# Kernel tuning notes

Hardware: AMD Instinct MI355X
Metric: run time of the kernel (lower is better)

Reference implementation:

```python
import jax, jax.numpy as jnp
import numpy as np

N = 50000
E = 1600000
IN_DIM = 128
OUT_DIM = 128
HEADS = 4
C = OUT_DIM // HEADS  # per-head channels = 32
EDGE_DIM = 16
NEG_SLOPE = 0.2
LN_EPS = 1e-5


def setup_inputs() -> dict:
    key = jax.random.key(0)
    ks = jax.random.split(key, 12)
    s = 1.0 / np.sqrt(IN_DIM)
    return {
        "x": jax.random.normal(ks[0], (N, IN_DIM), dtype=jnp.float32),
        "edge_index": jax.random.randint(ks[1], (2, E), 0, N, dtype=jnp.int64),
        "edge_attr": jax.random.normal(ks[2], (E, EDGE_DIM), dtype=jnp.float32),
        # GATv2Conv params
        "W_l": jax.random.normal(ks[3], (IN_DIM, HEADS * C), dtype=jnp.float32) * s,
        "b_l": jnp.zeros((HEADS * C,), dtype=jnp.float32),
        "W_r": jax.random.normal(ks[4], (IN_DIM, HEADS * C), dtype=jnp.float32) * s,
        "b_r": jnp.zeros((HEADS * C,), dtype=jnp.float32),
        "W_e": jax.random.normal(ks[5], (EDGE_DIM, HEADS * C), dtype=jnp.float32) * (1.0 / np.sqrt(EDGE_DIM)),
        "att": jax.random.normal(ks[6], (HEADS, C), dtype=jnp.float32) * (1.0 / np.sqrt(C)),
        "conv_bias": jnp.zeros((HEADS * C,), dtype=jnp.float32),
        # LayerNorm params
        "gamma": jnp.ones((OUT_DIM,), dtype=jnp.float32),
        "beta": jnp.zeros((OUT_DIM,), dtype=jnp.float32),
    }


def _gat_layer(x, edge_index, edge_attr, W_l, b_l, W_r, b_r, W_e, att, conv_bias, gamma, beta):
    src, dst = edge_index[0], edge_index[1]
    # linear projections -> [N, H, C] / [E, H, C]
    x_l = (x @ W_l + b_l).reshape(N, HEADS, C)  # source-side
    x_r = (x @ W_r + b_r).reshape(N, HEADS, C)  # target-side
    e_f = (edge_attr @ W_e).reshape(E, HEADS, C)
    # GATv2 attention logits per edge/head
    z = x_l[src] + x_r[dst] + e_f                      # [E, H, C]
    z = jnp.where(z >= 0, z, NEG_SLOPE * z)            # LeakyReLU(0.2)
    logits = jnp.einsum('ehc,hc->eh', z, att)          # [E, H]
    # segment softmax over incoming edges of each target node
    m = jax.ops.segment_max(logits, dst, num_segments=N)          # [N, H]
    m = jnp.where(jnp.isfinite(m), m, 0.0)
    ex = jnp.exp(logits - m[dst])                                  # [E, H]
    denom = jax.ops.segment_sum(ex, dst, num_segments=N)          # [N, H]
    alpha = ex / (denom[dst] + 1e-16)                              # [E, H]
    # weighted message aggregation (dropout on alpha skipped: eval mode)
    msg = x_l[src] * alpha[:, :, None]                             # [E, H, C]
    out = jax.ops.segment_sum(msg, dst, num_segments=N)           # [N, H, C]
    out = out.reshape(N, HEADS * C) + conv_bias                    # concat heads
    # LayerNorm -> ReLU -> (dropout: identity) -> residual (Identity since in==out)
    mu = jnp.mean(out, axis=-1, keepdims=True)
    var = jnp.mean(jnp.square(out - mu), axis=-1, keepdims=True)
    out = (out - mu) * jax.lax.rsqrt(var + LN_EPS) * gamma + beta
    out = jax.nn.relu(out)
    return out + x


def reference(x, edge_index, edge_attr, W_l, b_l, W_r, b_r, W_e, att, conv_bias, gamma, beta):
    return _gat_layer(x, edge_index, edge_attr, W_l, b_l, W_r, b_r, W_e, att, conv_bias, gamma, beta)
```

## Files before the change

kernel.cpp:

```cpp
#include <hip/hip_runtime.h>
#include <hip/hip_bf16.h>

#define NPB 32
#define PAD 64
#define OVF_CAP 4096

typedef float f32x2 __attribute__((ext_vector_type(2)));

__device__ __forceinline__ float b2f(__hip_bfloat16 v) { return __bfloat162float(v); }
__device__ __forceinline__ float ldf(const void* p, long i, int f32) {
    return f32 ? ((const float*)p)[i] : b2f(((const __hip_bfloat16*)p)[i]);
}
__device__ __forceinline__ float bflo(unsigned u) { union { unsigned i; float f; } v; v.i = u << 16; return v.f; }
__device__ __forceinline__ float bfhi(unsigned u) { union { unsigned i; float f; } v; v.i = u & 0xffff0000u; return v.f; }
__device__ __forceinline__ float2 ldf2(const void* p, long i2, int f32) {
    if (f32) return ((const float2*)p)[i2];
    unsigned u = ((const unsigned*)p)[i2];
    return make_float2(bflo(u), bfhi(u));
}
__device__ __forceinline__ int ldi(const int* p, long i, int i32) {
    return i32 ? p[i] : p[2 * i];
}
__device__ __forceinline__ int rfl(int v) { return __builtin_amdgcn_readfirstlane(v); }

template <int CTRL>
__device__ __forceinline__ float dpp_add(float v) {
    int s = __builtin_amdgcn_update_dpp(0, __float_as_int(v), CTRL, 0xF, 0xF, true);
    return v + __int_as_float(s);
}

__global__ void zero_i(int* __restrict__ a, long n, int* __restrict__ dt)
{
    long i = (long)blockIdx.x * 256 + threadIdx.x;
    long stride = (long)gridDim.x * 256;
    for (; i < n; i += stride) a[i] = 0;
    if (blockIdx.x == 0 && threadIdx.x == 0 && dt) { dt[0] = 0; dt[1] = 0; }
}

__global__ void fail_stamp(float* __restrict__ out, float code)
{
    if (threadIdx.x == 0 && blockIdx.x == 0) out[0] = code;
}

__global__ void detect_kernel(const void* __restrict__ x, const int* __restrict__ ei,
                              int* __restrict__ dt, int E_)
{
    int t = threadIdx.x;
    const unsigned short* xb = (const unsigned short*)x;
    int f32 = 0;
    for (int i = t; i < 4096; i += 256) {
        int ex = (xb[i] >> 7) & 0xFF;
        if (ex > 140) f32 = 1;
    }
    if (f32) atomicOr(&dt[0], 1);
    int nz = 0;
    for (int i = t; i < 2048; i += 256) nz |= ei[2 * i + 1];
    if (nz) atomicOr(&dt[1], 1);
}

__global__ __launch_bounds__(128) void gemm_xlr(
    const void* __restrict__ x,
    const void* __restrict__ Wl, const void* __restrict__ bl,
    const void* __restrict__ Wr, const void* __restrict__ br,
    const int* __restrict__ dt,
    __hip_bfloat16* __restrict__ xl, __hip_bfloat16* __restrict__ xr, int n)
{
    __shared__ float xs[NPB][128];
    int f32 = dt[0];
    int t = threadIdx.x;
    int n0 = blockIdx.x * NPB;
    for (int j = 0; j < NPB; ++j) {
        int node = n0 + j;
        xs[j][t] = (node < n) ? ldf(x, (long)node * 128 + t, f32) : 0.f;
    }
    __syncthreads();
    f32x2 acc[NPB];
#pragma unroll
    for (int j = 0; j < NPB; ++j) acc[j] = (f32x2){0.f, 0.f};
    for (int k = 0; k < 128; ++k) {
        f32x2 wlr = { ldf(Wl, k * 128 + t, f32), ldf(Wr, k * 128 + t, f32) };
#pragma unroll
        for (int j = 0; j < NPB; ++j) {
            f32x2 xv = { xs[j][k], xs[j][k] };
            acc[j] = __builtin_elementwise_fma(xv, wlr, acc[j]);
        }
    }
    float blv = ldf(bl, t, f32);
    float brv = ldf(br, t, f32);
    for (int j = 0; j < NPB; ++j) {
        int node = n0 + j;
        if (node < n) {
            xl[(long)node * 128 + t] = __float2bfloat16(acc[j].x + blv);
            xr[(long)node * 128 + t] = __float2bfloat16(acc[j].y + brv);
        }
    }
}

__global__ __launch_bounds__(256) void scatter_pad(
    const int* __restrict__ ei, const int* __restrict__ dt,
    int* __restrict__ cnt, int* __restrict__ ovfcnt,
    int2* __restrict__ se_pad, int4* __restrict__ ovf, int E_, int N_)
{
    long e = (long)blockIdx.x * 256 + threadIdx.x;
    if (e >= E_) return;
    int i32 = dt[1];
    int s = ldi(ei, e, i32);
    int d = ldi(ei, E_ + e, i32);
    if ((unsigned)s < (unsigned)N_ && (unsigned)d < (unsigned)N_) {
        int k = atomicAdd(&cnt[d], 1);
        if (k < PAD) se_pad[(long)d * PAD + k] = make_int2(s, (int)e);
        else {
            int o = atomicAdd(ovfcnt, 1);
            if (o < OVF_CAP) ovf[o] = make_int4(d, s, (int)e, 0);
        }
    }
}

#define EDGE_PRE(UC)  f32x2 z = { bflo(UC) + w0, bfhi(UC) + w1 };
#define EFMA(val, idx) z = __builtin_elementwise_fma((f32x2){(val), (val)}, W[idx], z);
#define EDGE_POST(UC) \
    z = __builtin_elementwise_max(z, z * 0.2f);                    \
    float vv = fmaf(z.y, attv.y, z.x * attv.x);                                        \
    vv = dpp_add<0xB1>(vv);  vv = dpp_add<0x4E>(vv);                                   \
    vv = dpp_add<0x124>(vv); vv = dpp_add<0x128>(vv);            \
    float exv = __expf(vv);                                                            \
    acc = __builtin_elementwise_fma((f32x2){exv, exv},                                 \
                                    (f32x2){bflo(UC), bfhi(UC)}, acc);                 \
    den += exv;
#define EDGE16(E0, E1, UC) { EDGE_PRE(UC)                                              \
    EFMA(bflo(E0.x), 0)  EFMA(bfhi(E0.x), 1)  EFMA(bflo(E0.y), 2)  EFMA(bfhi(E0.y), 3) \
    EFMA(bflo(E0.z), 4)  EFMA(bfhi(E0.z), 5)  EFMA(bflo(E0.w), 6)  EFMA(bfhi(E0.w), 7) \
    EFMA(bflo(E1.x), 8)  EFMA(bfhi(E1.x), 9)  EFMA(bflo(E1.y), 10) EFMA(bfhi(E1.y), 11)\
    EFMA(bflo(E1.z), 12) EFMA(bfhi(E1.z), 13) EFMA(bflo(E1.w), 14) EFMA(bfhi(E1.w), 15)\
    EDGE_POST(UC) }
#define EDGE32(F0, F1, F2, F3, UC) { EDGE_PRE(UC)                                      \
    EFMA(F0.x, 0)  EFMA(F0.y, 1)  EFMA(F0.z, 2)  EFMA(F0.w, 3)                          \
    EFMA(F1.x, 4)  EFMA(F1.y, 5)  EFMA(F1.z, 6)  EFMA(F1.w, 7)                          \
    EFMA(F2.x, 8)  EFMA(F2.y, 9)  EFMA(F2.z, 10) EFMA(F2.w, 11)                         \
    EFMA(F3.x, 12) EFMA(F3.y, 13) EFMA(F3.z, 14) EFMA(F3.w, 15)                         \
    EDGE_POST(UC) }

template <int F32>
__device__ __forceinline__ void node_run(
    const int* __restrict__ cnt, const int2* __restrict__ se_pad,
    const int4* __restrict__ ovf, const int* __restrict__ ovfcnt,
    const void* __restrict__ ea, const void* __restrict__ We, const void* __restrict__ att,
    const unsigned* __restrict__ xlu, const unsigned* __restrict__ xru,
    const void* __restrict__ cb, const void* __restrict__ gamma,
    const void* __restrict__ beta, const void* __restrict__ x,
    float* __restrict__ out, int N_)
{
    int w = threadIdx.x >> 6, j = threadIdx.x & 63;
    int n = blockIdx.x * 4 + w;
    if (n >= N_) return;

    f32x2 W[16];
#pragma unroll
    for (int k = 0; k < 16; ++k) {
        float2 v = ldf2(We, (long)k * 64 + j, F32);
        W[k] = (f32x2){v.x, v.y};
    }
    float2 attv = ldf2(att, j, F32);
    float2 cbv  = ldf2(cb, j, F32);
    float2 gv   = ldf2(gamma, j, F32);
    float2 bv   = ldf2(beta, j, F32);

    int deg = cnt[n];
    int m = deg < PAD ? deg : PAD;
    long base = (long)n * PAD;
    unsigned urow = xru[(long)n * 64 + j];
    float w0 = bflo(urow), w1 = bfhi(urow);
    f32x2 acc = {0.f, 0.f};
    float den = 0.f;

    if (m > 0) {
        if (F32) {
            int2 se0 = se_pad[base];
            int sA = rfl(se0.x), eA = rfl(se0.y);
            unsigned uA = xlu[((long)sA << 6) + j];
            const float4* qa = (const float4*)ea + (long)eA * 4;
            float4 f0 = qa[0], f1 = qa[1], f2 = qa[2], f3 = qa[3];
            int2 seB = se_pad[base + (m > 1 ? 1 : 0)];
            for (int k = 0; k < m; ++k) {
                int2 seC = se_pad[base + (k + 2 < m ? k + 2 : m - 1)];
                int sB = rfl(seB.x), eB = rfl(seB.y);
                unsigned uB = xlu[((long)sB << 6) + j];
                const float4* qb = (const float4*)ea + (long)eB * 4;
                float4 g0 = qb[0], g1 = qb[1], g2 = qb[2], g3 = qb[3];
                EDGE32(f0, f1, f2, f3, uA)
                seB = seC; uA = uB; f0 = g0; f1 = g1; f2 = g2; f3 = g3;
            }
        } else {
            int2 se0 = se_pad[base];
            int sA = rfl(se0.x), eA = rfl(se0.y);
            unsigned uA = xlu[((long)sA << 6) + j];
            const uint4* qa = (const uint4*)ea + (long)eA * 2;
            uint4 a0 = qa[0], a1 = qa[1];
            int2 seB = se_pad[base + (m > 1 ? 1 : 0)];
            for (int k = 0; k < m; ++k) {
                int2 seC = se_pad[base + (k + 2 < m ? k + 2 : m - 1)];
                int sB = rfl(seB.x), eB = rfl(seB.y);
                unsigned uB = xlu[((long)sB << 6) + j];
                const uint4* qb = (const uint4*)ea + (long)eB * 2;
                uint4 b0 = qb[0], b1 = qb[1];
                EDGE16(a0, a1, uA)
                seB = seC; uA = uB; a0 = b0; a1 = b1;
            }
        }
    }
    if (deg > PAD) {
        int oc = *ovfcnt; if (oc > OVF_CAP) oc = OVF_CAP;
        for (int o = 0; o < oc; ++o) {
            int4 v4 = ovf[o];
            if (rfl(v4.x) != n) continue;
            int sO = rfl(v4.y); long eO = rfl(v4.z);
            unsigned uO = xlu[((long)sO << 6) + j];
            if (F32) {
                const float4* qr = (const float4*)ea + eO * 4;
                float4 f0 = qr[0], f1 = qr[1], f2 = qr[2], f3 = qr[3];
                EDGE32(f0, f1, f2, f3, uO)
            } else {
                const uint4* qr = (const uint4*)ea + eO * 2;
                uint4 a0 = qr[0], a1 = qr[1];
                EDGE16(a0, a1, uO)
            }
        }
    }

    float rden = 1.f / (den + 1e-16f);
    float o0 = acc.x * rden + cbv.x;
    float o1 = acc.y * rden + cbv.y;

    float s = o0 + o1;
#pragma unroll
    for (int o = 1; o < 64; o <<= 1) s += __shfl_xor(s, o, 64);
    float mu = s * (1.f / 128.f);
    float d0 = o0 - mu, d1 = o1 - mu;
    float vs = d0 * d0 + d1 * d1;
#pragma unroll
    for (int o = 1; o < 64; o <<= 1) vs += __shfl_xor(vs, o, 64);
    float rs = rsqrtf(vs * (1.f / 128.f) + 1e-5f);
    float2 xv = ldf2(x, (long)n * 64 + j, F32);
    float y0 = fmaxf(d0 * rs * gv.x + bv.x, 0.f) + xv.x;
    float y1 = fmaxf(d1 * rs * gv.y + bv.y, 0.f) + xv.y;
    *(float2*)(out + (long)n * 128 + 2 * j) = make_float2(y0, y1);
}

__global__ __launch_bounds__(256, 4) void node_fused(
    const int* __restrict__ cnt, const int2* __restrict__ se_pad,
    const int4* __restrict__ ovf, const int* __restrict__ ovfcnt,
    const void* __restrict__ ea, const void* __restrict__ We, const void* __restrict__ att,
    const __hip_bfloat16* __restrict__ xl, const __hip_bfloat16* __restrict__ xr,
    const void* __restrict__ cb, const void* __restrict__ gamma,
    const void* __restrict__ beta, const void* __restrict__ x,
    const int* __restrict__ dt, float* __restrict__ out, int N_)
{
    const unsigned* xlu = (const unsigned*)xl;
    const unsigned* xru = (const unsigned*)xr;
    if (dt[0])
        node_run<1>(cnt, se_pad, ovf, ovfcnt, ea, We, att, xlu, xru,
                    cb, gamma, beta, x, out, N_);
    else
        node_run<0>(cnt, se_pad, ovf, ovfcnt, ea, We, att, xlu, xru,
                    cb, gamma, beta, x, out, N_);
}

extern "C" void kernel_launch(void* const* d_in, const int* in_sizes, int n_in,
                              void* d_out, int out_size, void* d_ws, size_t ws_size,
                              hipStream_t stream) {
    const void* x     = d_in[0];
    const int*  ei    = (const int*)d_in[1];
    const void* ea    = d_in[2];
    const void* Wl    = d_in[3];
    const void* bl    = d_in[4];
    const void* Wr    = d_in[5];
    const void* br    = d_in[6];
    const void* We    = d_in[7];
    const void* att   = d_in[8];
    const void* cb    = d_in[9];
    const void* gamma = d_in[10];
    const void* beta  = d_in[11];
    float* out = (float*)d_out;

    const int N_ = in_sizes[0] / 128;
    const int E_ = in_sizes[2] / 16;

    size_t need = 0;
    auto sz = [&](size_t b) { size_t r = need; need += (b + 255) & ~(size_t)255; return r; };
    size_t o_xl   = sz((size_t)N_ * 128 * 2);
    size_t o_xr   = sz((size_t)N_ * 128 * 2);
    size_t o_cnt  = sz((size_t)(N_ + 8) * 4);
    size_t o_dt   = sz(256);
    size_t o_se   = sz((size_t)N_ * PAD * 8);
    size_t o_ovf  = sz((size_t)OVF_CAP * 16);

    if (need > ws_size) {
        fail_stamp<<<1, 64, 0, stream>>>(out, 16384.f);
        return;
    }
    char* p = (char*)d_ws;
    __hip_bfloat16* xl   = (__hip_bfloat16*)(p + o_xl);
    __hip_bfloat16* xr   = (__hip_bfloat16*)(p + o_xr);
    int*   cnt           = (int*)(p + o_cnt);
    int*   ovfcnt        = cnt + N_;
    int*   dt            = (int*)(p + o_dt);
    int2*  se_pad        = (int2*)(p + o_se);
    int4*  ovf           = (int4*)(p + o_ovf);

    zero_i<<<256, 256, 0, stream>>>(cnt, N_ + 8, dt);
    detect_kernel<<<1, 256, 0, stream>>>(x, ei, dt, E_);
    gemm_xlr<<<(N_ + NPB - 1) / NPB, 128, 0, stream>>>(x, Wl, bl, Wr, br, dt, xl, xr, N_);
    scatter_pad<<<(E_ + 255) / 256, 256, 0, stream>>>(ei, dt, cnt, ovfcnt,
                                                      se_pad, ovf, E_, N_);
    node_fused<<<(N_ + 3) / 4, 256, 0, stream>>>(cnt, se_pad, ovf, ovfcnt, ea, We, att,
                                                 xl, xr, cb, gamma, beta, x, dt, out, N_);
}
```

Baseline: 620.8 us.

## Merge GEMM and edge scatter into one launch, deepen edge prefetch

Merges the x@W_l/W_r projection and the edge scatter into a single prep kernel, with separate blocks doing each task so they run concurrently. The GEMM now reads x straight from global memory instead of staging it in shared memory, and each thread computes one output column for 16 nodes. The scatter batches four edges per thread so their atomics are in flight together. The node loop prefetches edge data two edges ahead, and an asm constraint keeps W in registers, at the cost of higher register pressure.

```diff
diff --git a/kernel.cpp b/kernel.cpp
--- a/kernel.cpp
+++ b/kernel.cpp
@@ -1,7 +1,7 @@
 #include <hip/hip_runtime.h>
 #include <hip/hip_bf16.h>
 
-#define NPB 32
+#define GJB 16
 #define PAD 64
 #define OVF_CAP 4096
 
@@ -58,61 +58,90 @@
     if (nz) atomicOr(&dt[1], 1);
 }
 
-__global__ __launch_bounds__(128) void gemm_xlr(
+template <int F32>
+__device__ __forceinline__ void gemm_body(
     const void* __restrict__ x,
     const void* __restrict__ Wl, const void* __restrict__ bl,
     const void* __restrict__ Wr, const void* __restrict__ br,
-    const int* __restrict__ dt,
-    __hip_bfloat16* __restrict__ xl, __hip_bfloat16* __restrict__ xr, int n)
-{
-    __shared__ float xs[NPB][128];
-    int f32 = dt[0];
+    __hip_bfloat16* __restrict__ xl, __hip_bfloat16* __restrict__ xr,
+    int n, int blk)
+{
     int t = threadIdx.x;
-    int n0 = blockIdx.x * NPB;
-    for (int j = 0; j < NPB; ++j) {
+    int half = t >> 7, c = t & 127;
+    const void* W  = half ? Wr : Wl;
+    const void* bb = half ? br : bl;
+    __hip_bfloat16* dst = half ? xr : xl;
+    int n0 = blk * GJB;
+    float acc[GJB];
+#pragma unroll
+    for (int j = 0; j < GJB; ++j) acc[j] = 0.f;
+    for (int k0 = 0; k0 < 128; k0 += 4) {
+        float w0 = ldf(W, (long)(k0 + 0) * 128 + c, F32);
+        float w1 = ldf(W, (long)(k0 + 1) * 128 + c, F32);
+        float w2 = ldf(W, (long)(k0 + 2) * 128 + c, F32);
+        float w3 = ldf(W, (long)(k0 + 3) * 128 + c, F32);
+#pragma unroll
+        for (int j = 0; j < GJB; ++j) {
+            int node = n0 + j; if (node >= n) node = n - 1;
+            float x0, x1, x2, x3;
+            if (F32) {
+                float4 v = *(const float4*)((const float*)x + (long)node * 128 + k0);
+                x0 = v.x; x1 = v.y; x2 = v.z; x3 = v.w;
+            } else {
+                uint2 v = *(const uint2*)((const unsigned short*)x + (long)node * 128 + k0);
+                x0 = bflo(v.x); x1 = bfhi(v.x); x2 = bflo(v.y); x3 = bfhi(v.y);
+            }
+            acc[j] = fmaf(x3, w3, fmaf(x2, w2, fmaf(x1, w1, fmaf(x0, w0, acc[j]))));
+        }
+    }
+    float bv = ldf(bb, c, F32);
+    for (int j = 0; j < GJB; ++j) {
         int node = n0 + j;
-        xs[j][t] = (node < n) ? ldf(x, (long)node * 128 + t, f32) : 0.f;
-    }
-    __syncthreads();
-    f32x2 acc[NPB];
-#pragma unroll
-    for (int j = 0; j < NPB; ++j) acc[j] = (f32x2){0.f, 0.f};
-    for (int k = 0; k < 128; ++k) {
-        f32x2 wlr = { ldf(Wl, k * 128 + t, f32), ldf(Wr, k * 128 + t, f32) };
-#pragma unroll
-        for (int j = 0; j < NPB; ++j) {
-            f32x2 xv = { xs[j][k], xs[j][k] };
-            acc[j] = __builtin_elementwise_fma(xv, wlr, acc[j]);
-        }
-    }
-    float blv = ldf(bl, t, f32);
-    float brv = ldf(br, t, f32);
-    for (int j = 0; j < NPB; ++j) {
-        int node = n0 + j;
-        if (node < n) {
-            xl[(long)node * 128 + t] = __float2bfloat16(acc[j].x + blv);
-            xr[(long)node * 128 + t] = __float2bfloat16(acc[j].y + brv);
-        }
-    }
-}
-
-__global__ __launch_bounds__(256) void scatter_pad(
+        if (node < n) dst[(long)node * 128 + c] = __float2bfloat16(acc[j] + bv);
+    }
+}
+
+__global__ __launch_bounds__(256) void prep_kernel(
+    const void* __restrict__ x,
+    const void* __restrict__ Wl, const void* __restrict__ bl,
+    const void* __restrict__ Wr, const void* __restrict__ br,
     const int* __restrict__ ei, const int* __restrict__ dt,
+    __hip_bfloat16* __restrict__ xl, __hip_bfloat16* __restrict__ xr,
     int* __restrict__ cnt, int* __restrict__ ovfcnt,
-    int2* __restrict__ se_pad, int4* __restrict__ ovf, int E_, int N_)
-{
-    long e = (long)blockIdx.x * 256 + threadIdx.x;
-    if (e >= E_) return;
-    int i32 = dt[1];
-    int s = ldi(ei, e, i32);
-    int d = ldi(ei, E_ + e, i32);
-    if ((unsigned)s < (unsigned)N_ && (unsigned)d < (unsigned)N_) {
-        int k = atomicAdd(&cnt[d], 1);
-        if (k < PAD) se_pad[(long)d * PAD + k] = make_int2(s, (int)e);
-        else {
-            int o = atomicAdd(ovfcnt, 1);
-            if (o < OVF_CAP) ovf[o] = make_int4(d, s, (int)e, 0);
-        }
+    int2* __restrict__ se_pad, int4* __restrict__ ovf,
+    int n, int E_, int gScat)
+{
+    if ((int)blockIdx.x < gScat) {
+        int i32 = dt[1];
+        long e0 = (long)blockIdx.x * 1024 + threadIdx.x;
+        int sA[4], dA[4], eA[4], kA[4];
+#pragma unroll
+        for (int i = 0; i < 4; ++i) {
+            long e = e0 + i * 256;
+            int s = -1, d = -1;
+            if (e < E_) {
+                s = ldi(ei, e, i32);
+                d = ldi(ei, E_ + e, i32);
+                if (!((unsigned)s < (unsigned)n && (unsigned)d < (unsigned)n)) d = -1;
+            }
+            sA[i] = s; dA[i] = d; eA[i] = (int)e;
+        }
+#pragma unroll
+        for (int i = 0; i < 4; ++i)
+            kA[i] = (dA[i] >= 0) ? atomicAdd(&cnt[dA[i]], 1) : 0;
+#pragma unroll
+        for (int i = 0; i < 4; ++i) {
+            if (dA[i] < 0) continue;
+            if (kA[i] < PAD) se_pad[(long)dA[i] * PAD + kA[i]] = make_int2(sA[i], eA[i]);
+            else {
+                int o = atomicAdd(ovfcnt, 1);
+                if (o < OVF_CAP) ovf[o] = make_int4(dA[i], sA[i], eA[i], 0);
+            }
+        }
+    } else {
+        int blk = blockIdx.x - gScat;
+        if (dt[0]) gemm_body<1>(x, Wl, bl, Wr, br, xl, xr, n, blk);
+        else       gemm_body<0>(x, Wl, bl, Wr, br, xl, xr, n, blk);
     }
 }
 
@@ -140,6 +169,12 @@
     EFMA(F3.x, 12) EFMA(F3.y, 13) EFMA(F3.z, 14) EFMA(F3.w, 15)                         \
     EDGE_POST(UC) }
 
+#define PIN_W asm volatile("" : "+v"(W[0]), "+v"(W[1]), "+v"(W[2]),  "+v"(W[3]),       \
+    "+v"(W[4]),  "+v"(W[5]),  "+v"(W[6]),  "+v"(W[7]),  "+v"(W[8]),  "+v"(W[9]),       \
+    "+v"(W[10]), "+v"(W[11]), "+v"(W[12]), "+v"(W[13]), "+v"(W[14]), "+v"(W[15]))
+
+#define SLOT(k) (base + ((k) < m ? (k) : m - 1))
+
 template <int F32>
 __device__ __forceinline__ void node_run(
     const int* __restrict__ cnt, const int2* __restrict__ se_pad,
@@ -175,36 +210,48 @@
 
     if (m > 0) {
         if (F32) {
-            int2 se0 = se_pad[base];
-            int sA = rfl(se0.x), eA = rfl(se0.y);
+            int2 s0 = se_pad[SLOT(0)];
+            int sA = rfl(s0.x), eA = rfl(s0.y);
             unsigned uA = xlu[((long)sA << 6) + j];
             const float4* qa = (const float4*)ea + (long)eA * 4;
             float4 f0 = qa[0], f1 = qa[1], f2 = qa[2], f3 = qa[3];
-            int2 seB = se_pad[base + (m > 1 ? 1 : 0)];
+            int2 s1 = se_pad[SLOT(1)];
+            int sB = rfl(s1.x), eB = rfl(s1.y);
+            unsigned uB = xlu[((long)sB << 6) + j];
+            const float4* qb = (const float4*)ea + (long)eB * 4;
+            float4 g0 = qb[0], g1 = qb[1], g2 = qb[2], g3 = qb[3];
             for (int k = 0; k < m; ++k) {
-                int2 seC = se_pad[base + (k + 2 < m ? k + 2 : m - 1)];
-                int sB = rfl(seB.x), eB = rfl(seB.y);
-                unsigned uB = xlu[((long)sB << 6) + j];
-                const float4* qb = (const float4*)ea + (long)eB * 4;
-                float4 g0 = qb[0], g1 = qb[1], g2 = qb[2], g3 = qb[3];
+                int2 sc = se_pad[SLOT(k + 2)];
+                int sC = rfl(sc.x), eC = rfl(sc.y);
+                unsigned uC = xlu[((long)sC << 6) + j];
+                const float4* qc = (const float4*)ea + (long)eC * 4;
+                float4 h0 = qc[0], h1 = qc[1], h2 = qc[2], h3 = qc[3];
+                PIN_W;
                 EDGE32(f0, f1, f2, f3, uA)
-                seB = seC; uA = uB; f0 = g0; f1 = g1; f2 = g2; f3 = g3;
+                uA = uB; f0 = g0; f1 = g1; f2 = g2; f3 = g3;
+                uB = uC; g0 = h0; g1 = h1; g2 = h2; g3 = h3;
             }
         } else {
-            int2 se0 = se_pad[base];
-            int sA = rfl(se0.x), eA = rfl(se0.y);
+            int2 s0 = se_pad[SLOT(0)];
+            int sA = rfl(s0.x), eA = rfl(s0.y);
             unsigned uA = xlu[((long)sA << 6) + j];
             const uint4* qa = (const uint4*)ea + (long)eA * 2;
             uint4 a0 = qa[0], a1 = qa[1];
-            int2 seB = se_pad[base + (m > 1 ? 1 : 0)];
+            int2 s1 = se_pad[SLOT(1)];
+            int sB = rfl(s1.x), eB = rfl(s1.y);
+            unsigned uB = xlu[((long)sB << 6) + j];
+            const uint4* qb = (const uint4*)ea + (long)eB * 2;
+            uint4 b0 = qb[0], b1 = qb[1];
             for (int k = 0; k < m; ++k) {
-                int2 seC = se_pad[base + (k + 2 < m ? k + 2 : m - 1)];
-                int sB = rfl(seB.x), eB = rfl(seB.y);
-                unsigned uB = xlu[((long)sB << 6) + j];
-                const uint4* qb = (const uint4*)ea + (long)eB * 2;
-                uint4 b0 = qb[0], b1 = qb[1];
+                int2 sc = se_pad[SLOT(k + 2)];
+                int sC = rfl(sc.x), eC = rfl(sc.y);
+                unsigned uC = xlu[((long)sC << 6) + j];
+                const uint4* qc = (const uint4*)ea + (long)eC * 2;
+                uint4 c0 = qc[0], c1 = qc[1];
+                PIN_W;
                 EDGE16(a0, a1, uA)
-                seB = seC; uA = uB; a0 = b0; a1 = b1;
+                uA = uB; a0 = b0; a1 = b1;
+                uB = uC; b0 = c0; b1 = c1;
             }
         }
     }
@@ -309,9 +356,11 @@
 
     zero_i<<<256, 256, 0, stream>>>(cnt, N_ + 8, dt);
     detect_kernel<<<1, 256, 0, stream>>>(x, ei, dt, E_);
-    gemm_xlr<<<(N_ + NPB - 1) / NPB, 128, 0, stream>>>(x, Wl, bl, Wr, br, dt, xl, xr, N_);
-    scatter_pad<<<(E_ + 255) / 256, 256, 0, stream>>>(ei, dt, cnt, ovfcnt,
-                                                      se_pad, ovf, E_, N_);
+    int gScat = (E_ + 1023) / 1024;
+    int gGemm = (N_ + GJB - 1) / GJB;
+    prep_kernel<<<gScat + gGemm, 256, 0, stream>>>(x, Wl, bl, Wr, br, ei, dt, xl, xr,
+                                                   cnt, ovfcnt, se_pad, ovf,
+                                                   N_, E_, gScat);
     node_fused<<<(N_ + 3) / 4, 256, 0, stream>>>(cnt, se_pad, ovf, ovfcnt, ea, We, att,
                                                  xl, xr, cb, gamma, beta, x, dt, out, N_);
 }
```

After: 707.2 us. +13.9%, slower.
